# Kernel tuning notes

Measured on AMD Instinct MI355X. Metric: run time of the kernel, lower is better.

## Reference

```python
import jax, jax.numpy as jnp
from jax import lax
import numpy as np

DN = ('NCHW', 'OIHW', 'NCHW')
LEAKY_SLOPE = 0.01  # torch nn.LeakyReLU default


def conv(x, w, b=None, stride=1, pad=0):
    y = lax.conv_general_dilated(x, w, (stride, stride), [(pad, pad), (pad, pad)],
                                 dimension_numbers=DN)
    return y if b is None else y + b[None, :, None, None]


def conv_transpose2d(x, w, b):
    # torch ConvTranspose2d(k=4, s=2, p=1); w layout (Cin, Cout, 4, 4)
    wf = jnp.transpose(jnp.flip(w, (2, 3)), (1, 0, 2, 3))  # -> OIHW
    y = lax.conv_general_dilated(x, wf, (1, 1), [(2, 2), (2, 2)],
                                 lhs_dilation=(2, 2), dimension_numbers=DN)
    return y + b[None, :, None, None]


def residual_stack(x, rw3, rw1):
    # 6 ResidualLayers: x + conv1x1(relu(conv3x3(x))), both convs bias-free
    for i in range(rw3.shape[0]):
        h = jax.nn.relu(conv(x, rw3[i], pad=1))
        x = x + conv(h, rw1[i])
    return x


def vector_quantize(latents, codebook):
    # latents: [B, D, H, W] -> NHWC
    lat = jnp.transpose(latents, (0, 2, 3, 1))
    B, H, W, D = lat.shape
    flat = lat.reshape(-1, D)  # [N, D]
    # pairwise squared distances [N, K]
    dist = (jnp.sum(flat ** 2, axis=1, keepdims=True)
            + jnp.sum(codebook ** 2, axis=1)
            - 2.0 * flat @ codebook.T)
    inds = jnp.argmin(dist, axis=1)            # [N]
    q = codebook[inds].reshape(B, H, W, D)     # gather == one-hot matmul
    commitment_loss = jnp.mean((lax.stop_gradient(q) - lat) ** 2)
    embedding_loss = jnp.mean((q - lax.stop_gradient(lat)) ** 2)
    q_st = lat + lax.stop_gradient(q - lat)    # straight-through
    return jnp.transpose(q_st, (0, 3, 1, 2)), embedding_loss, commitment_loss


def setup_inputs() -> dict:
    key = jax.random.key(0)
    ks = iter(jax.random.split(key, 32))
    B, C, S = 16, 3, 128
    H0, H1 = 128, 256          # hidden_dims
    D, K = 64, 512             # embedding_dim, num_embeddings
    n_res = 6

    def w(shape, scale=0.05):
        return (jax.random.normal(next(ks), shape, dtype=jnp.float32) * scale)

    inp = {
        'x': jax.random.normal(next(ks), (B, C, S, S), dtype=jnp.float32),
        # encoder
        'ew0': w((H0, C, 4, 4)), 'eb0': jnp.zeros((H0,), jnp.float32),
        'ew1': w((H1, H0, 4, 4)), 'eb1': jnp.zeros((H1,), jnp.float32),
        'ew2': w((H1, H1, 3, 3)), 'eb2': jnp.zeros((H1,), jnp.float32),
        'erw3': w((n_res, H1, H1, 3, 3)),
        'erw1': w((n_res, H1, H1, 1, 1)),
        'ew3': w((D, H1, 1, 1)), 'eb3': jnp.zeros((D,), jnp.float32),
        # codebook, uniform(-1/K, 1/K) as in torch init
        'codebook': jax.random.uniform(next(ks), (K, D), jnp.float32, -1.0 / K, 1.0 / K),
        # decoder
        'dw0': w((H1, D, 3, 3)), 'db0': jnp.zeros((H1,), jnp.float32),
        'drw3': w((n_res, H1, H1, 3, 3)),
        'drw1': w((n_res, H1, H1, 1, 1)),
        'tw0': w((H1, H0, 4, 4)), 'tb0': jnp.zeros((H0,), jnp.float32),
        'tw1': w((H0, C, 4, 4)), 'tb1': jnp.zeros((C,), jnp.float32),
    }
    return inp


def reference(x, ew0, eb0, ew1, eb1, ew2, eb2, erw3, erw1, ew3, eb3,
              codebook, dw0, db0, drw3, drw1, tw0, tb0, tw1, tb1):
    lrelu = lambda t: jax.nn.leaky_relu(t, LEAKY_SLOPE)
    # encoder: two stride-2 downsamples, conv3x3, 6 residuals, 1x1 -> D
    h = lrelu(conv(x, ew0, eb0, stride=2, pad=1))   # [B,128,64,64]
    h = lrelu(conv(h, ew1, eb1, stride=2, pad=1))   # [B,256,32,32]
    h = lrelu(conv(h, ew2, eb2, stride=1, pad=1))
    h = residual_stack(h, erw3, erw1)
    h = lrelu(h)
    z = lrelu(conv(h, ew3, eb3))                    # [B,64,32,32]
    # vector quantization
    q, embedding_loss, commitment_loss = vector_quantize(z, codebook)
    # decoder
    d = lrelu(conv(q, dw0, db0, stride=1, pad=1))   # [B,256,32,32]
    d = residual_stack(d, drw3, drw1)
    d = lrelu(d)
    d = lrelu(conv_transpose2d(d, tw0, tb0))        # [B,128,64,64]
    recons = jnp.tanh(conv_transpose2d(d, tw1, tb1))  # [B,3,128,128]
    return recons, embedding_loss, commitment_loss
```

## Files before the change

### kernel.cpp

```cpp
#include <hip/hip_runtime.h>
#include <math.h>


typedef __attribute__((ext_vector_type(8))) short bf16x8;
typedef __attribute__((ext_vector_type(4))) float f32x4;

__device__ __forceinline__ float bf2f(short s) {
    unsigned u = ((unsigned)(unsigned short)s) << 16;
    return __builtin_bit_cast(float, u);
}
__device__ __forceinline__ unsigned short f2bfu(float f) {
    unsigned u = __builtin_bit_cast(unsigned, f);
    u = (u + 0x7fff + ((u >> 16) & 1)) >> 16;
    return (unsigned short)u;
}
__device__ __forceinline__ short f2bf(float f) { return (short)f2bfu(f); }

template<int ACT>
__device__ __forceinline__ float actf(float v) {
    if (ACT == 1) return fmaxf(v, 0.f);
    if (ACT == 2) return v > 0.f ? v : 0.01f * v;
    return v;
}

__device__ __forceinline__ void gload_lds16(const void* g, void* l) {
    __builtin_amdgcn_global_load_lds(
        (const __attribute__((address_space(1))) unsigned int*)g,
        (__attribute__((address_space(3))) unsigned int*)l, 16, 0, 0);
}

__device__ __forceinline__ int fof(int r) { return (r & 3) ^ ((r >> 2) & 3); }

#define WAITV(N) asm volatile("s_waitcnt vmcnt(" #N ")" ::: "memory")

__global__ __launch_bounds__(256) void prep_perm_k(const float* __restrict__ src,
        short* __restrict__ dst, int COUT, int CIN, int T, int total) {
    int i = blockIdx.x * 256 + threadIdx.x;
    if (i >= total) return;
    int ic = i % CIN; int r = i / CIN;
    int oc = r % COUT; r /= COUT;
    int t = r % T; int c = r / T;
    dst[i] = f2bf(src[(((size_t)c * COUT + oc) * CIN + ic) * T + t]);
}

__global__ __launch_bounds__(256) void prep_tw0_k(const float* __restrict__ src,
        short* __restrict__ dst) {
    int i = blockIdx.x * 256 + threadIdx.x;
    if (i >= 4 * 4 * 128 * 256) return;
    int ic = i & 255; int r = i >> 8;
    int oc = r & 127; r >>= 7;
    int tap = r & 3; int par = r >> 2;
    int py = par >> 1, px = par & 1, my = tap >> 1, mx = tap & 1;
    int ky = 2 * my + (py ^ 1), kx = 2 * mx + (px ^ 1);
    dst[i] = f2bf(src[(((size_t)ic * 128 + oc) * 4 + ky) * 4 + kx]);
}

template<int CIN, int NTAPS, int TAPPAT, int SM, int INW, int OUTACT,
         bool HASB, bool FUSE>
__global__ __launch_bounds__(512, 1) void rconv_k(
        const short* __restrict__ in, const short* __restrict__ Wp,
        const float* __restrict__ bias, const short* __restrict__ W1p,
        short* __restrict__ outp) {
    constexpr int CH64 = (CIN >= 128) ? CIN / 64 : 1;
    constexpr int LG2 = (CH64 == 4) ? 2 : (CH64 == 2) ? 1 : 0;
    constexpr int ST = NTAPS * CH64;
    __shared__ short sLds[FUSE ? 77824 : 61440];
    const int tid = threadIdx.x;
    const int lane = tid & 63, wv = tid >> 6;
    const int wr = wv >> 2, wc = wv & 3;
    const int pix0 = blockIdx.x * 64;
    const int l15 = lane & 15, hi = lane >> 4;
    const int sl = (hi ^ fof(l15)) * 8;

    const int arow = (tid >> 2) & 63, akk = tid >> 8, aslot = tid & 3;
    const short* Aptr;
    {
        int pixa = pix0 + arow;
        int ba = pixa >> 10, Ya = (pixa >> 5) & 31, Xa = pixa & 31;
        Aptr = in + (size_t)((ba * INW + SM * Ya + 2) * INW + (SM * Xa + 2)) * CIN
                  + akk * 32 + (aslot ^ fof(arow)) * 8;
    }
    const short* Bptr[4];
#pragma unroll
    for (int j = 0; j < 4; j++) {
        int gb = tid + 512 * j;
        int kkb = gb >> 10, oc = (gb >> 2) & 255, slb = gb & 3;
        Bptr[j] = Wp + (size_t)oc * CIN + kkb * 32 + ((slb ^ fof(oc)) * 8);
    }

    auto stage = [&](int s, int bi) {
        int t = s >> LG2;
        int c0 = (s & (CH64 - 1)) * 64;
        int rof, cof;
        if (TAPPAT == 1) { rof = t / 3 - 1; cof = t % 3 - 1; }
        else             { rof = (t >> 2) - 1; cof = (t & 3) - 1; }
        int aoff = (rof * INW + cof) * CIN + c0;
        int woff = t * (256 * CIN) + c0;
        char* L = (char*)sLds + bi * 40960;
        gload_lds16(Aptr + aoff, L + tid * 16);
#pragma unroll
        for (int j = 0; j < 4; j++)
            gload_lds16(Bptr[j] + woff, L + 8192 + (tid + 512 * j) * 16);
    };

    f32x4 acc[2][4];
#pragma unroll
    for (int mi = 0; mi < 2; mi++)
#pragma unroll
        for (int ni = 0; ni < 4; ni++) acc[mi][ni] = f32x4{0.f, 0.f, 0.f, 0.f};

    stage(0, 0);
    stage(1, 1);
    int bi = 0;
    for (int s = 0; s < ST; ++s) {
        if (s < ST - 1) { WAITV(5); } else { WAITV(0); }
        __builtin_amdgcn_s_barrier();
        int nx = bi + 2; if (nx >= 3) nx -= 3;
        if (s + 2 < ST) stage(s + 2, nx);
        const short* L = sLds + bi * 20480;
        const short* LB = L + 4096;
        bf16x8 af[2][2], bfr[4][2];
#pragma unroll
        for (int kk = 0; kk < 2; kk++) {
#pragma unroll
            for (int mi = 0; mi < 2; mi++)
                af[mi][kk] = *(const bf16x8*)(L + kk * 2048
                    + (wr * 32 + mi * 16 + l15) * 32 + sl);
#pragma unroll
            for (int ni = 0; ni < 4; ni++)
                bfr[ni][kk] = *(const bf16x8*)(LB + kk * 8192
                    + (wc * 64 + ni * 16 + l15) * 32 + sl);
        }
        __builtin_amdgcn_s_setprio(1);
#pragma unroll
        for (int kk = 0; kk < 2; kk++)
#pragma unroll
            for (int mi = 0; mi < 2; mi++)
#pragma unroll
                for (int ni = 0; ni < 4; ni++)
                    acc[mi][ni] = __builtin_amdgcn_mfma_f32_16x16x32_bf16(
                        af[mi][kk], bfr[ni][kk], acc[mi][ni], 0, 0, 0);
        __builtin_amdgcn_s_setprio(0);
        bi = (bi == 2) ? 0 : bi + 1;
    }

    if (!FUSE) {
#pragma unroll
        for (int mi = 0; mi < 2; mi++)
#pragma unroll
            for (int r = 0; r < 4; r++) {
                int lrow = wr * 32 + mi * 16 + hi * 4 + r;
                int pix = pix0 + lrow;
                int b = pix >> 10, Y = (pix >> 5) & 31, X = pix & 31;
                size_t base = (((size_t)b * 36 + Y + 2) * 36 + X + 2) * 256;
#pragma unroll
                for (int ni = 0; ni < 4; ni++) {
                    int col = wc * 64 + ni * 16 + l15;
                    float v = acc[mi][ni][r];
                    if (HASB) v += bias[col];
                    outp[base + col] = f2bf(actf<OUTACT>(v));
                }
            }
        return;
    }

    short* H = sLds + 61440;
#pragma unroll
    for (int mi = 0; mi < 2; mi++)
#pragma unroll
        for (int r = 0; r < 4; r++) {
            int lrow = wr * 32 + mi * 16 + hi * 4 + r;
            int frow = fof(lrow);
#pragma unroll
            for (int ni = 0; ni < 4; ni++) {
                int col = wc * 64 + ni * 16 + l15;
                H[((col >> 5) * 64 + lrow) * 32 + (((col >> 3) & 3) ^ frow) * 8
                  + (col & 7)] = f2bf(fmaxf(acc[mi][ni][r], 0.f));
            }
        }

    const short* W1ptr[4];
#pragma unroll
    for (int j = 0; j < 4; j++) {
        int gb = tid + 512 * j;
        int kkb = gb >> 10, oc = (gb >> 2) & 255, slb = gb & 3;
        W1ptr[j] = W1p + (size_t)oc * 256 + kkb * 32 + ((slb ^ fof(oc)) * 8);
    }
    auto stage2 = [&](int s2, int bb) {
        char* L = (char*)sLds + bb * 40960 + 8192;
#pragma unroll
        for (int j = 0; j < 4; j++)
            gload_lds16(W1ptr[j] + s2 * 64, L + (tid + 512 * j) * 16);
    };
    stage2(0, 0);
    stage2(1, 1);
    __syncthreads();

    f32x4 acc2[2][4];
#pragma unroll
    for (int mi = 0; mi < 2; mi++)
#pragma unroll
        for (int ni = 0; ni < 4; ni++) acc2[mi][ni] = f32x4{0.f, 0.f, 0.f, 0.f};

    for (int s2 = 0; s2 < 4; ++s2) {
        if (s2 < 3) { WAITV(4); } else { WAITV(0); }
        __builtin_amdgcn_s_barrier();
        if (s2 == 0) stage2(2, 2);
        if (s2 == 1) stage2(3, 0);
        const short* LB = sLds + ((s2 < 3) ? s2 : 0) * 20480 + 4096;
        bf16x8 af2[2][2], bf2r[4][2];
#pragma unroll
        for (int kk = 0; kk < 2; kk++) {
            int ck = s2 * 2 + kk;
#pragma unroll
            for (int mi = 0; mi < 2; mi++)
                af2[mi][kk] = *(const bf16x8*)(H
                    + (ck * 64 + wr * 32 + mi * 16 + l15) * 32 + sl);
#pragma unroll
            for (int ni = 0; ni < 4; ni++)
                bf2r[ni][kk] = *(const bf16x8*)(LB + kk * 8192
                    + (wc * 64 + ni * 16 + l15) * 32 + sl);
        }
        __builtin_amdgcn_s_setprio(1);
#pragma unroll
        for (int kk = 0; kk < 2; kk++)
#pragma unroll
            for (int mi = 0; mi < 2; mi++)
#pragma unroll
                for (int ni = 0; ni < 4; ni++)
                    acc2[mi][ni] = __builtin_amdgcn_mfma_f32_16x16x32_bf16(
                        af2[mi][kk], bf2r[ni][kk], acc2[mi][ni], 0, 0, 0);
        __builtin_amdgcn_s_setprio(0);
    }
#pragma unroll
    for (int mi = 0; mi < 2; mi++)
#pragma unroll
        for (int r = 0; r < 4; r++) {
            int lrow = wr * 32 + mi * 16 + hi * 4 + r;
            int pix = pix0 + lrow;
            int b = pix >> 10, Y = (pix >> 5) & 31, X = pix & 31;
            size_t base = (((size_t)b * 36 + Y + 2) * 36 + X + 2) * 256;
#pragma unroll
            for (int ni = 0; ni < 4; ni++) {
                int col = wc * 64 + ni * 16 + l15;
                float v = acc2[mi][ni][r] + bf2f(in[base + col]);
                outp[base + col] = f2bf(actf<OUTACT>(v));
            }
        }
}

template<int CIN, int COUT, int NTAPS, int TAPPAT, int SM, int INW,
         int OUTACT, bool RES, bool HASB, int OUTMODE, int BN>
__global__ __launch_bounds__(256) void gconv_k(
        const short* __restrict__ in, const short* __restrict__ Wp,
        const float* __restrict__ bias, const short* __restrict__ res,
        void* __restrict__ outp) {
    constexpr int KCH = CIN / 32;
    constexpr int LG = (KCH == 8) ? 3 : (KCH == 4) ? 2 : (KCH == 2) ? 1 : 0;
    constexpr int ST = NTAPS * KCH;
    constexpr int NF = BN / 32;
    constexpr int WN = BN / 2;
    __shared__ short sA[3 * 128 * 32];
    __shared__ short sB[3 * BN * 32];
    const int tid = threadIdx.x;
    const int lane = tid & 63, wv = tid >> 6;
    const int wr = wv >> 1, wc = wv & 1;
    const int pix0 = blockIdx.x * 128;
    const int oc0 = blockIdx.y * BN;
    int py = 0, px = 0;
    if (TAPPAT == 3) {
        int par = blockIdx.z;
        py = par >> 1; px = par & 1;
        Wp += (size_t)par * NTAPS * COUT * CIN;
    }

    const int sp = tid >> 2;
    const int fsp = fof(sp);
    const int swz = ((tid & 3) ^ fsp) * 8;
    int rbA[2];
#pragma unroll
    for (int rd = 0; rd < 2; rd++) {
        int pix = pix0 + sp + rd * 64;
        int b = pix >> 10, Y = (pix >> 5) & 31, X = pix & 31;
        rbA[rd] = ((b * INW + SM * Y + 2) * INW + (SM * X + 2)) * CIN + swz;
    }
    const int wb0 = (oc0 + sp) * CIN + swz;
    const int wb1 = (oc0 + sp + 64) * CIN + swz;

    f32x4 acc[4][NF];
#pragma unroll
    for (int i = 0; i < 4; i++)
#pragma unroll
        for (int j = 0; j < NF; j++) acc[i][j] = f32x4{0.f, 0.f, 0.f, 0.f};

    const int sslot = ((lane >> 4) ^ fof(lane & 15)) * 8;
    const int abase = (wr * 64 + (lane & 15)) * 32 + sslot;
    const int bbase = (wc * WN + (lane & 15)) * 32 + sslot;

    auto stage = [&](int s, int biq) {
        int t = s >> LG, c = s & (KCH - 1);
        int rof, cof;
        if (TAPPAT == 0) { rof = 0; cof = 0; }
        else if (TAPPAT == 1) { rof = t / 3 - 1; cof = t % 3 - 1; }
        else if (TAPPAT == 2) { rof = t / 4 - 1; cof = t % 4 - 1; }
        else { int my = t >> 1, mx = t & 1;
               rof = (py == 0) ? -my : 1 - my;
               cof = (px == 0) ? -mx : 1 - mx; }
        const int tapoff = (rof * INW + cof) * CIN + c * 32;
        char* a = (char*)sA + biq * 8192;
        char* b = (char*)sB + biq * (BN * 64);
        const short* wt = Wp + (size_t)t * COUT * CIN + c * 32;
        gload_lds16(in + rbA[0] + tapoff, a + tid * 16);
        gload_lds16(in + rbA[1] + tapoff, a + 4096 + tid * 16);
        gload_lds16(wt + wb0, b + tid * 16);
        if (BN == 128) gload_lds16(wt + wb1, b + 4096 + tid * 16);
    };

    stage(0, 0);
    stage(1, 1);
    int cur = 0;
    for (int s = 0; s < ST; ++s) {
        if (s < ST - 1) {
            if (BN == 128) { WAITV(4); } else { WAITV(3); }
        } else {
            WAITV(0);
        }
        __builtin_amdgcn_s_barrier();
        int nxt = cur + 2; if (nxt >= 3) nxt -= 3;
        if (s + 2 < ST) stage(s + 2, nxt);
        const short* a = sA + cur * 4096;
        const short* b = sB + cur * (BN * 32);
        bf16x8 af[4], bfm[NF];
#pragma unroll
        for (int mi = 0; mi < 4; mi++)
            af[mi] = *(const bf16x8*)(a + abase + mi * 512);
#pragma unroll
        for (int ni = 0; ni < NF; ni++)
            bfm[ni] = *(const bf16x8*)(b + bbase + ni * 512);
        __builtin_amdgcn_s_setprio(1);
#pragma unroll
        for (int mi = 0; mi < 4; mi++)
#pragma unroll
            for (int ni = 0; ni < NF; ni++)
                acc[mi][ni] = __builtin_amdgcn_mfma_f32_16x16x32_bf16(
                    af[mi], bfm[ni], acc[mi][ni], 0, 0, 0);
        __builtin_amdgcn_s_setprio(0);
        cur = (cur == 2) ? 0 : cur + 1;
    }
#pragma unroll
    for (int mi = 0; mi < 4; mi++) {
#pragma unroll
        for (int r = 0; r < 4; r++) {
            int pix = pix0 + wr * 64 + mi * 16 + (lane >> 4) * 4 + r;
            int b = pix >> 10, Y = (pix >> 5) & 31, X = pix & 31;
            size_t rowoff = 0;
            if (OUTMODE == 0)
                rowoff = (((size_t)b * 36 + Y + 2) * 36 + X + 2) * COUT;
            else if (OUTMODE == 2)
                rowoff = (((size_t)b * 68 + 2 * Y + py + 2) * 68 + 2 * X + px + 2) * 128;
#pragma unroll
            for (int ni = 0; ni < NF; ni++) {
                int col = oc0 + wc * WN + ni * 16 + (lane & 15);
                float v = acc[mi][ni][r];
                if (HASB) v += bias[col];
                if (OUTMODE == 1) {
                    ((float*)outp)[(size_t)pix * COUT + col] = actf<OUTACT>(v);
                } else {
                    size_t off = rowoff + col;
                    if (RES) v += bf2f(res[off]);
                    ((short*)outp)[off] = f2bf(actf<OUTACT>(v));
                }
            }
        }
    }
}

__global__ __launch_bounds__(256) void conv0_k(const float* __restrict__ x,
        const float* __restrict__ W, const float* __restrict__ bias,
        short* __restrict__ P0) {
    __shared__ float sIn[3 * 18 * 66];
    __shared__ float sW[48 * 32];
    int b = blockIdx.z, ocg = blockIdx.y, tile = blockIdx.x;
    int y0 = (tile >> 1) * 8, x0 = (tile & 1) * 32;
    int tid = threadIdx.x;
    for (int t = tid; t < 1536; t += 256) {
        int k = t >> 5, oc = t & 31;
        sW[t] = W[(size_t)(ocg * 32 + oc) * 48 + k];
    }
    for (int t = tid; t < 3 * 18 * 66; t += 256) {
        int ic = t / 1188; int rem = t - ic * 1188;
        int ry = rem / 66, rx = rem - ry * 66;
        int iy = 2 * y0 - 1 + ry, ix = 2 * x0 - 1 + rx;
        float v = 0.f;
        if ((unsigned)iy < 128u && (unsigned)ix < 128u)
            v = x[((size_t)b * 3 + ic) * 16384 + iy * 128 + ix];
        sIn[t] = v;
    }
    __syncthreads();
    int r = tid >> 5, cx = tid & 31;
    float acc[32];
#pragma unroll
    for (int o = 0; o < 32; o++) acc[o] = 0.f;
#pragma unroll
    for (int ic = 0; ic < 3; ic++) {
#pragma unroll
        for (int k = 0; k < 16; k++) {
            int ky = k >> 2, kx = k & 3;
            float xv = sIn[ic * 1188 + (2 * r + ky) * 66 + 2 * cx + kx];
            const float4* wp = (const float4*)(sW + (ic * 16 + k) * 32);
#pragma unroll
            for (int q = 0; q < 8; q++) {
                float4 w = wp[q];
                acc[4 * q + 0] += w.x * xv; acc[4 * q + 1] += w.y * xv;
                acc[4 * q + 2] += w.z * xv; acc[4 * q + 3] += w.w * xv;
            }
        }
    }
    size_t base = (((size_t)b * 68 + y0 + r + 2) * 68 + x0 + cx + 2) * 128 + ocg * 32;
#pragma unroll
    for (int q = 0; q < 16; q++) {
        float v0 = actf<2>(acc[2 * q] + bias[ocg * 32 + 2 * q]);
        float v1 = actf<2>(acc[2 * q + 1] + bias[ocg * 32 + 2 * q + 1]);
        ((int*)(P0 + base))[q] = (int)f2bfu(v0) | ((int)f2bfu(v1) << 16);
    }
}

__global__ __launch_bounds__(256) void vq_argmin_k(const float* __restrict__ zr,
        const float* __restrict__ cb, int* __restrict__ ind) {
    __shared__ short sZ[2][128 * 32];
    __shared__ short sC[2][128 * 32];
    __shared__ float sN[128];
    const int tid = threadIdx.x;
    const int lane = tid & 63, wv = tid >> 6;
    const int pos0 = blockIdx.x * 128;
#pragma unroll
    for (int it = 0; it < 4; ++it) {
        int task = tid + it * 256;
        int row = task >> 3, kq = task & 7;
        const float4* zp = (const float4*)(zr + (size_t)(pos0 + row) * 64 + kq * 8);
        float4 v0 = zp[0], v1 = zp[1];
        int slot = ((kq & 3) ^ fof(row)) * 8;
        short tmp[8] = {f2bf(v0.x), f2bf(v0.y), f2bf(v0.z), f2bf(v0.w),
                        f2bf(v1.x), f2bf(v1.y), f2bf(v1.z), f2bf(v1.w)};
        *(bf16x8*)&sZ[kq >> 2][row * 32 + slot] = *(bf16x8*)tmp;
    }
    const int sslot = ((lane >> 4) ^ fof(lane & 15)) * 8;
    const int l15 = lane & 15;
    float best[2][4]; int bidx[2][4];
#pragma unroll
    for (int mi = 0; mi < 2; mi++)
#pragma unroll
        for (int r = 0; r < 4; r++) { best[mi][r] = INFINITY; bidx[mi][r] = 0; }
    for (int ch = 0; ch < 4; ++ch) {
        __syncthreads();
#pragma unroll
        for (int it = 0; it < 4; ++it) {
            int task = tid + it * 256;
            int row = task >> 3, kq = task & 7;
            const float4* cp = (const float4*)(cb + (size_t)(ch * 128 + row) * 64 + kq * 8);
            float4 v0 = cp[0], v1 = cp[1];
            int slot = ((kq & 3) ^ fof(row)) * 8;
            short tmp[8] = {f2bf(v0.x), f2bf(v0.y), f2bf(v0.z), f2bf(v0.w),
                            f2bf(v1.x), f2bf(v1.y), f2bf(v1.z), f2bf(v1.w)};
            *(bf16x8*)&sC[kq >> 2][row * 32 + slot] = *(bf16x8*)tmp;
        }
        if (tid < 128) {
            const float4* cp = (const float4*)(cb + (size_t)(ch * 128 + tid) * 64);
            float s = 0.f;
#pragma unroll
            for (int q = 0; q < 16; q++) {
                float4 v = cp[q];
                s += v.x * v.x + v.y * v.y + v.z * v.z + v.w * v.w;
            }
            sN[tid] = s;
        }
        __syncthreads();
        f32x4 acc[2][8];
#pragma unroll
        for (int mi = 0; mi < 2; mi++)
#pragma unroll
            for (int ni = 0; ni < 8; ni++) acc[mi][ni] = f32x4{0.f, 0.f, 0.f, 0.f};
#pragma unroll
        for (int kc = 0; kc < 2; ++kc) {
            bf16x8 za[2], ca[8];
#pragma unroll
            for (int mi = 0; mi < 2; mi++)
                za[mi] = *(const bf16x8*)&sZ[kc][(wv * 32 + mi * 16 + l15) * 32 + sslot];
#pragma unroll
            for (int ni = 0; ni < 8; ni++)
                ca[ni] = *(const bf16x8*)&sC[kc][(ni * 16 + l15) * 32 + sslot];
#pragma unroll
            for (int mi = 0; mi < 2; mi++)
#pragma unroll
                for (int ni = 0; ni < 8; ni++)
                    acc[mi][ni] = __builtin_amdgcn_mfma_f32_16x16x32_bf16(
                        za[mi], ca[ni], acc[mi][ni], 0, 0, 0);
        }
#pragma unroll
        for (int mi = 0; mi < 2; mi++)
#pragma unroll
            for (int ni = 0; ni < 8; ni++) {
                float nrm = sN[ni * 16 + l15];
                int idx = ch * 128 + ni * 16 + l15;
#pragma unroll
                for (int r = 0; r < 4; r++) {
                    float sc = nrm - 2.f * acc[mi][ni][r];
                    if (sc < best[mi][r]) { best[mi][r] = sc; bidx[mi][r] = idx; }
                }
            }
    }
#pragma unroll
    for (int m = 1; m < 16; m <<= 1) {
#pragma unroll
        for (int mi = 0; mi < 2; mi++)
#pragma unroll
            for (int r = 0; r < 4; r++) {
                float os = __shfl_xor(best[mi][r], m);
                int   oi = __shfl_xor(bidx[mi][r], m);
                if (os < best[mi][r] || (os == best[mi][r] && oi < bidx[mi][r])) {
                    best[mi][r] = os; bidx[mi][r] = oi;
                }
            }
    }
    if (l15 == 0) {
        int g = lane >> 4;
#pragma unroll
        for (int mi = 0; mi < 2; mi++)
#pragma unroll
            for (int r = 0; r < 4; r++)
                ind[pos0 + wv * 32 + mi * 16 + g * 4 + r] = bidx[mi][r];
    }
}

__global__ __launch_bounds__(256) void vq_gather_k(const float* __restrict__ zr,
        const float* __restrict__ cb, const int* __restrict__ ind,
        short* __restrict__ q, float* __restrict__ part) {
    int pos = blockIdx.x * 256 + threadIdx.x;
    int b = pos >> 10, hw = pos & 1023, y = hw >> 5, xx = hw & 31;
    int idx = ind[pos];
    const float4* cp = (const float4*)(cb + (size_t)idx * 64);
    const float4* zp = (const float4*)(zr + (size_t)pos * 64);
    size_t qb = (((size_t)b * 36 + y + 2) * 36 + xx + 2) * 64;
    float sum = 0.f;
#pragma unroll
    for (int d4 = 0; d4 < 16; d4++) {
        float4 c = cp[d4], z = zp[d4];
        float dx = c.x - z.x, dy = c.y - z.y, dz = c.z - z.z, dw = c.w - z.w;
        sum += dx * dx + dy * dy + dz * dz + dw * dw;
        ((int*)(q + qb))[2 * d4] = (int)f2bfu(c.x) | ((int)f2bfu(c.y) << 16);
        ((int*)(q + qb))[2 * d4 + 1] = (int)f2bfu(c.z) | ((int)f2bfu(c.w) << 16);
    }
#pragma unroll
    for (int m = 1; m < 64; m <<= 1) sum += __shfl_xor(sum, m);
    __shared__ float sred[4];
    int lane = threadIdx.x & 63, wvv = threadIdx.x >> 6;
    if (lane == 0) sred[wvv] = sum;
    __syncthreads();
    if (threadIdx.x == 0)
        part[blockIdx.x] = sred[0] + sred[1] + sred[2] + sred[3];
}

__global__ void finalize_k(const float* __restrict__ part, float* __restrict__ out) {
    if (threadIdx.x == 0) {
        float s = 0.f;
        for (int k = 0; k < 64; k++) s += part[k];
        float m = s / 1048576.f;
        out[786432] = m;
        out[786433] = m;
    }
}

__global__ __launch_bounds__(256) void tw1_k(const short* __restrict__ in,
        const float* __restrict__ W, const float* __restrict__ bias,
        float* __restrict__ out) {
    __shared__ float sW[16 * 128 * 4];
    int b = blockIdx.y, y0 = blockIdx.x * 8;
    int tid = threadIdx.x;
    for (int t = tid; t < 2048; t += 256) {
        int k = t >> 7, ic = t & 127;
        float4 v;
        v.x = W[((size_t)ic * 3 + 0) * 16 + k];
        v.y = W[((size_t)ic * 3 + 1) * 16 + k];
        v.z = W[((size_t)ic * 3 + 2) * 16 + k];
        v.w = 0.f;
        *(float4*)&sW[t * 4] = v;
    }
    __syncthreads();
    int r = tid >> 5, g = tid & 31;
    int oy = y0 + r, py = oy & 1, Y = oy >> 1, pxp = g & 1;
    float acc[4][3];
#pragma unroll
    for (int p = 0; p < 4; p++)
#pragma unroll
        for (int o = 0; o < 3; o++) acc[p][o] = 0.f;
#pragma unroll
    for (int my = 0; my < 2; my++) {
        int iy = Y + ((py == 0) ? -my : 1 - my) + 2;
        const short* rowp = in + (((size_t)b * 68 + iy) * 68) * 128;
        int ky = 2 * my + (py ^ 1);
#pragma unroll
        for (int mx = 0; mx < 2; mx++) {
            int kx = 2 * mx + (pxp ^ 1);
            int cof = ((pxp == 0) ? -mx : 1 - mx) + 2;
            const float* wbase = &sW[((ky * 4 + kx) * 128) * 4];
            const short* pptr[4];
#pragma unroll
            for (int p = 0; p < 4; p++) {
                int X = ((g + 32 * p) >> 1) + cof;
                pptr[p] = rowp + (size_t)X * 128;
            }
            for (int icb = 0; icb < 16; icb++) {
                bf16x8 v[4];
#pragma unroll
                for (int p = 0; p < 4; p++)
                    v[p] = *(const bf16x8*)(pptr[p] + icb * 8);
#pragma unroll
                for (int j = 0; j < 8; j++) {
                    float4 w = *(const float4*)&wbase[(icb * 8 + j) * 4];
#pragma unroll
                    for (int p = 0; p < 4; p++) {
                        float xv = bf2f(v[p][j]);
                        acc[p][0] += w.x * xv;
                        acc[p][1] += w.y * xv;
                        acc[p][2] += w.z * xv;
                    }
                }
            }
        }
    }
#pragma unroll
    for (int p = 0; p < 4; p++) {
        int ox = g + 32 * p;
#pragma unroll
        for (int o = 0; o < 3; o++)
            out[(((size_t)b * 3 + o) << 14) + oy * 128 + ox] =
                tanhf(acc[p][o] + bias[o]);
    }
}

extern "C" void kernel_launch(void* const* d_in, const int* in_sizes, int n_in,
                              void* d_out, int out_size, void* d_ws, size_t ws_size,
                              hipStream_t stream) {
    const float* x    = (const float*)d_in[0];
    const float* ew0  = (const float*)d_in[1];
    const float* eb0  = (const float*)d_in[2];
    const float* ew1  = (const float*)d_in[3];
    const float* eb1  = (const float*)d_in[4];
    const float* ew2  = (const float*)d_in[5];
    const float* eb2  = (const float*)d_in[6];
    const float* erw3 = (const float*)d_in[7];
    const float* erw1 = (const float*)d_in[8];
    const float* ew3  = (const float*)d_in[9];
    const float* eb3  = (const float*)d_in[10];
    const float* cbk  = (const float*)d_in[11];
    const float* dw0  = (const float*)d_in[12];
    const float* db0  = (const float*)d_in[13];
    const float* drw3 = (const float*)d_in[14];
    const float* drw1 = (const float*)d_in[15];
    const float* tw0  = (const float*)d_in[16];
    const float* tb0  = (const float*)d_in[17];
    const float* tw1  = (const float*)d_in[18];
    const float* tb1  = (const float*)d_in[19];
    float* out = (float*)d_out;

    short* S = (short*)d_ws;
    short* P0  = S;
    short* PB  = P0 + 9469952;
    short* PC  = PB + 5308416;
    short* Pq  = PC + 5308416;
    short* Wp1 = Pq + 1327104;
    short* We2 = Wp1 + 524288;
    short* Wer3 = We2 + 589824;
    short* We11 = Wer3 + 3538944;
    short* Wz   = We11 + 393216;
    short* Wd0  = Wz + 16384;
    short* Wdr3 = Wd0 + 147456;
    short* Wdr1 = Wdr3 + 3538944;
    short* Wt0  = Wdr1 + 393216;
    float* F   = (float*)(S + 31080448);
    float* Zr  = F;
    float* PART = Zr + 1048576;
    int*   IND = (int*)(PART + 64);

    hipMemsetAsync(d_ws, 0, (size_t)21413888 * 2, stream);

    auto gp = [](int n) { return dim3((n + 255) / 256); };
    prep_perm_k<<<gp(524288), 256, 0, stream>>>(ew1, Wp1, 256, 128, 16, 524288);
    prep_perm_k<<<gp(589824), 256, 0, stream>>>(ew2, We2, 256, 256, 9, 589824);
    prep_perm_k<<<gp(3538944), 256, 0, stream>>>(erw3, Wer3, 256, 256, 9, 3538944);
    prep_perm_k<<<gp(393216), 256, 0, stream>>>(erw1, We11, 256, 256, 1, 393216);
    prep_perm_k<<<gp(16384), 256, 0, stream>>>(ew3, Wz, 64, 256, 1, 16384);
    prep_perm_k<<<gp(147456), 256, 0, stream>>>(dw0, Wd0, 256, 64, 9, 147456);
    prep_perm_k<<<gp(3538944), 256, 0, stream>>>(drw3, Wdr3, 256, 256, 9, 3538944);
    prep_perm_k<<<gp(393216), 256, 0, stream>>>(drw1, Wdr1, 256, 256, 1, 393216);
    prep_tw0_k<<<gp(524288), 256, 0, stream>>>(tw0, Wt0);

    conv0_k<<<dim3(16, 4, 16), 256, 0, stream>>>(x, ew0, eb0, P0);
    rconv_k<128, 16, 2, 2, 68, 2, true, false>
        <<<256, 512, 0, stream>>>(P0, Wp1, eb1, nullptr, PB);
    rconv_k<256, 9, 1, 1, 36, 2, true, false>
        <<<256, 512, 0, stream>>>(PB, We2, eb2, nullptr, PC);
    for (int i = 0; i < 6; i++) {
        short* inb  = (i & 1) ? PB : PC;
        short* outb = (i & 1) ? PC : PB;
        if (i < 5)
            rconv_k<256, 9, 1, 1, 36, 0, false, true>
                <<<256, 512, 0, stream>>>(inb, Wer3 + (size_t)i * 589824,
                    nullptr, We11 + (size_t)i * 65536, outb);
        else
            rconv_k<256, 9, 1, 1, 36, 2, false, true>
                <<<256, 512, 0, stream>>>(inb, Wer3 + (size_t)i * 589824,
                    nullptr, We11 + (size_t)i * 65536, outb);
    }
    gconv_k<256, 64, 1, 0, 1, 36, 2, false, true, 1, 64>
        <<<dim3(128, 1), 256, 0, stream>>>(PC, Wz, eb3, nullptr, Zr);

    vq_argmin_k<<<128, 256, 0, stream>>>(Zr, cbk, IND);
    vq_gather_k<<<64, 256, 0, stream>>>(Zr, cbk, IND, Pq, PART);

    rconv_k<64, 9, 1, 1, 36, 2, true, false>
        <<<256, 512, 0, stream>>>(Pq, Wd0, db0, nullptr, PC);
    for (int i = 0; i < 6; i++) {
        short* inb  = (i & 1) ? PB : PC;
        short* outb = (i & 1) ? PC : PB;
        if (i < 5)
            rconv_k<256, 9, 1, 1, 36, 0, false, true>
                <<<256, 512, 0, stream>>>(inb, Wdr3 + (size_t)i * 589824,
                    nullptr, Wdr1 + (size_t)i * 65536, outb);
        else
            rconv_k<256, 9, 1, 1, 36, 2, false, true>
                <<<256, 512, 0, stream>>>(inb, Wdr3 + (size_t)i * 589824,
                    nullptr, Wdr1 + (size_t)i * 65536, outb);
    }
    gconv_k<256, 128, 4, 3, 1, 36, 2, false, true, 2, 128>
        <<<dim3(128, 1, 4), 256, 0, stream>>>(PC, Wt0, tb0, nullptr, P0);
    tw1_k<<<dim3(16, 16), 256, 0, stream>>>(P0, tw1, tb1, out);

    finalize_k<<<1, 64, 0, stream>>>(PART, out);
}
```

Measured before the change: 632.1 us.

## Double rconv pixel tile to 128 rows and restructure conv0 per output row

```diff
diff --git a/kernel.cpp b/kernel.cpp
--- a/kernel.cpp
+++ b/kernel.cpp
@@ -32,6 +32,7 @@
 __device__ __forceinline__ int fof(int r) { return (r & 3) ^ ((r >> 2) & 3); }
 
 #define WAITV(N) asm volatile("s_waitcnt vmcnt(" #N ")" ::: "memory")
+#define LGKM0 asm volatile("s_waitcnt lgkmcnt(0)" ::: "memory")
 
 __global__ __launch_bounds__(256) void prep_perm_k(const float* __restrict__ src,
         short* __restrict__ dst, int COUT, int CIN, int T, int total) {
@@ -64,21 +65,21 @@
     constexpr int CH64 = (CIN >= 128) ? CIN / 64 : 1;
     constexpr int LG2 = (CH64 == 4) ? 2 : (CH64 == 2) ? 1 : 0;
     constexpr int ST = NTAPS * CH64;
-    __shared__ short sLds[FUSE ? 77824 : 61440];
+    __shared__ short sLds[73728];
     const int tid = threadIdx.x;
     const int lane = tid & 63, wv = tid >> 6;
     const int wr = wv >> 2, wc = wv & 3;
-    const int pix0 = blockIdx.x * 64;
+    const int pix0 = blockIdx.x * 128;
     const int l15 = lane & 15, hi = lane >> 4;
     const int sl = (hi ^ fof(l15)) * 8;
 
-    const int arow = (tid >> 2) & 63, akk = tid >> 8, aslot = tid & 3;
+    const int arow = tid >> 2, aslot = tid & 3;
     const short* Aptr;
     {
         int pixa = pix0 + arow;
         int ba = pixa >> 10, Ya = (pixa >> 5) & 31, Xa = pixa & 31;
         Aptr = in + (size_t)((ba * INW + SM * Ya + 2) * INW + (SM * Xa + 2)) * CIN
-                  + akk * 32 + (aslot ^ fof(arow)) * 8;
+                  + (aslot ^ fof(arow)) * 8;
     }
     const short* Bptr[4];
 #pragma unroll
@@ -95,17 +96,18 @@
         if (TAPPAT == 1) { rof = t / 3 - 1; cof = t % 3 - 1; }
         else             { rof = (t >> 2) - 1; cof = (t & 3) - 1; }
         int aoff = (rof * INW + cof) * CIN + c0;
+        char* L = (char*)sLds + bi * 49152;
+        gload_lds16(Aptr + aoff, L + tid * 16);
+        gload_lds16(Aptr + aoff + 32, L + 8192 + tid * 16);
         int woff = t * (256 * CIN) + c0;
-        char* L = (char*)sLds + bi * 40960;
-        gload_lds16(Aptr + aoff, L + tid * 16);
 #pragma unroll
         for (int j = 0; j < 4; j++)
-            gload_lds16(Bptr[j] + woff, L + 8192 + (tid + 512 * j) * 16);
+            gload_lds16(Bptr[j] + woff, L + 16384 + (tid + 512 * j) * 16);
     };
 
-    f32x4 acc[2][4];
-#pragma unroll
-    for (int mi = 0; mi < 2; mi++)
+    f32x4 acc[4][4];
+#pragma unroll
+    for (int mi = 0; mi < 4; mi++)
 #pragma unroll
         for (int ni = 0; ni < 4; ni++) acc[mi][ni] = f32x4{0.f, 0.f, 0.f, 0.f};
 
@@ -113,43 +115,41 @@
     stage(1, 1);
     int bi = 0;
     for (int s = 0; s < ST; ++s) {
-        if (s < ST - 1) { WAITV(5); } else { WAITV(0); }
+        if (s < ST - 1) { WAITV(6); } else { WAITV(0); }
         __builtin_amdgcn_s_barrier();
         int nx = bi + 2; if (nx >= 3) nx -= 3;
         if (s + 2 < ST) stage(s + 2, nx);
-        const short* L = sLds + bi * 20480;
-        const short* LB = L + 4096;
-        bf16x8 af[2][2], bfr[4][2];
+        const short* L = sLds + bi * 24576;
 #pragma unroll
         for (int kk = 0; kk < 2; kk++) {
-#pragma unroll
-            for (int mi = 0; mi < 2; mi++)
-                af[mi][kk] = *(const bf16x8*)(L + kk * 2048
-                    + (wr * 32 + mi * 16 + l15) * 32 + sl);
+            bf16x8 af[4], bfr[4];
+#pragma unroll
+            for (int mi = 0; mi < 4; mi++)
+                af[mi] = *(const bf16x8*)(L + kk * 4096
+                    + (wr * 64 + mi * 16 + l15) * 32 + sl);
 #pragma unroll
             for (int ni = 0; ni < 4; ni++)
-                bfr[ni][kk] = *(const bf16x8*)(LB + kk * 8192
+                bfr[ni] = *(const bf16x8*)(L + 8192 + kk * 8192
                     + (wc * 64 + ni * 16 + l15) * 32 + sl);
-        }
-        __builtin_amdgcn_s_setprio(1);
-#pragma unroll
-        for (int kk = 0; kk < 2; kk++)
-#pragma unroll
-            for (int mi = 0; mi < 2; mi++)
+            __builtin_amdgcn_s_setprio(1);
+#pragma unroll
+            for (int mi = 0; mi < 4; mi++)
 #pragma unroll
                 for (int ni = 0; ni < 4; ni++)
                     acc[mi][ni] = __builtin_amdgcn_mfma_f32_16x16x32_bf16(
-                        af[mi][kk], bfr[ni][kk], acc[mi][ni], 0, 0, 0);
-        __builtin_amdgcn_s_setprio(0);
+                        af[mi], bfr[ni], acc[mi][ni], 0, 0, 0);
+            __builtin_amdgcn_s_setprio(0);
+        }
+        LGKM0;
         bi = (bi == 2) ? 0 : bi + 1;
     }
 
     if (!FUSE) {
 #pragma unroll
-        for (int mi = 0; mi < 2; mi++)
+        for (int mi = 0; mi < 4; mi++)
 #pragma unroll
             for (int r = 0; r < 4; r++) {
-                int lrow = wr * 32 + mi * 16 + hi * 4 + r;
+                int lrow = wr * 64 + mi * 16 + hi * 4 + r;
                 int pix = pix0 + lrow;
                 int b = pix >> 10, Y = (pix >> 5) & 31, X = pix & 31;
                 size_t base = (((size_t)b * 36 + Y + 2) * 36 + X + 2) * 256;
@@ -164,21 +164,22 @@
         return;
     }
 
-    short* H = sLds + 61440;
-#pragma unroll
-    for (int mi = 0; mi < 2; mi++)
+    __builtin_amdgcn_s_barrier();
+    short* H = sLds;
+#pragma unroll
+    for (int mi = 0; mi < 4; mi++)
 #pragma unroll
         for (int r = 0; r < 4; r++) {
-            int lrow = wr * 32 + mi * 16 + hi * 4 + r;
+            int lrow = wr * 64 + mi * 16 + hi * 4 + r;
             int frow = fof(lrow);
 #pragma unroll
             for (int ni = 0; ni < 4; ni++) {
                 int col = wc * 64 + ni * 16 + l15;
-                H[((col >> 5) * 64 + lrow) * 32 + (((col >> 3) & 3) ^ frow) * 8
-                  + (col & 7)] = f2bf(fmaxf(acc[mi][ni][r], 0.f));
-            }
-        }
-
+                H[(((col >> 5) * 128) + lrow) * 32
+                  + ((((col >> 3) & 3) ^ frow) * 8) + (col & 7)] =
+                    f2bf(fmaxf(acc[mi][ni][r], 0.f));
+            }
+        }
     const short* W1ptr[4];
 #pragma unroll
     for (int j = 0; j < 4; j++) {
@@ -186,46 +187,46 @@
         int kkb = gb >> 10, oc = (gb >> 2) & 255, slb = gb & 3;
         W1ptr[j] = W1p + (size_t)oc * 256 + kkb * 32 + ((slb ^ fof(oc)) * 8);
     }
-    auto stage2 = [&](int s2, int bb) {
-        char* L = (char*)sLds + bb * 40960 + 8192;
+    auto stage2 = [&](int c) {
+        char* L = (char*)sLds + 65536 + (c & 1) * 32768;
 #pragma unroll
         for (int j = 0; j < 4; j++)
-            gload_lds16(W1ptr[j] + s2 * 64, L + (tid + 512 * j) * 16);
+            gload_lds16(W1ptr[j] + c * 64, L + (tid + 512 * j) * 16);
     };
-    stage2(0, 0);
-    stage2(1, 1);
-    __syncthreads();
-
-    f32x4 acc2[2][4];
-#pragma unroll
-    for (int mi = 0; mi < 2; mi++)
+    stage2(0);
+    stage2(1);
+    LGKM0;
+
+    f32x4 acc2[4][4];
+#pragma unroll
+    for (int mi = 0; mi < 4; mi++)
 #pragma unroll
         for (int ni = 0; ni < 4; ni++) acc2[mi][ni] = f32x4{0.f, 0.f, 0.f, 0.f};
 
     for (int s2 = 0; s2 < 4; ++s2) {
         if (s2 < 3) { WAITV(4); } else { WAITV(0); }
         __builtin_amdgcn_s_barrier();
-        if (s2 == 0) stage2(2, 2);
-        if (s2 == 1) stage2(3, 0);
-        const short* LB = sLds + ((s2 < 3) ? s2 : 0) * 20480 + 4096;
-        bf16x8 af2[2][2], bf2r[4][2];
+        const short* LB = sLds + 32768 + (s2 & 1) * 16384;
+        bf16x8 af2[4][2], bf2r[4][2];
 #pragma unroll
         for (int kk = 0; kk < 2; kk++) {
-            int ck = s2 * 2 + kk;
-#pragma unroll
-            for (int mi = 0; mi < 2; mi++)
+#pragma unroll
+            for (int mi = 0; mi < 4; mi++)
                 af2[mi][kk] = *(const bf16x8*)(H
-                    + (ck * 64 + wr * 32 + mi * 16 + l15) * 32 + sl);
+                    + ((s2 * 2 + kk) * 128 + wr * 64 + mi * 16 + l15) * 32 + sl);
 #pragma unroll
             for (int ni = 0; ni < 4; ni++)
                 bf2r[ni][kk] = *(const bf16x8*)(LB + kk * 8192
                     + (wc * 64 + ni * 16 + l15) * 32 + sl);
         }
+        LGKM0;
+        __builtin_amdgcn_s_barrier();
+        if (s2 < 2) stage2(s2 + 2);
         __builtin_amdgcn_s_setprio(1);
 #pragma unroll
         for (int kk = 0; kk < 2; kk++)
 #pragma unroll
-            for (int mi = 0; mi < 2; mi++)
+            for (int mi = 0; mi < 4; mi++)
 #pragma unroll
                 for (int ni = 0; ni < 4; ni++)
                     acc2[mi][ni] = __builtin_amdgcn_mfma_f32_16x16x32_bf16(
@@ -233,10 +234,10 @@
         __builtin_amdgcn_s_setprio(0);
     }
 #pragma unroll
-    for (int mi = 0; mi < 2; mi++)
+    for (int mi = 0; mi < 4; mi++)
 #pragma unroll
         for (int r = 0; r < 4; r++) {
-            int lrow = wr * 32 + mi * 16 + hi * 4 + r;
+            int lrow = wr * 64 + mi * 16 + hi * 4 + r;
             int pix = pix0 + lrow;
             int b = pix >> 10, Y = (pix >> 5) & 31, X = pix & 31;
             size_t base = (((size_t)b * 36 + Y + 2) * 36 + X + 2) * 256;
@@ -273,10 +274,8 @@
         py = par >> 1; px = par & 1;
         Wp += (size_t)par * NTAPS * COUT * CIN;
     }
-
     const int sp = tid >> 2;
-    const int fsp = fof(sp);
-    const int swz = ((tid & 3) ^ fsp) * 8;
+    const int swz = ((tid & 3) ^ fof(sp)) * 8;
     int rbA[2];
 #pragma unroll
     for (int rd = 0; rd < 2; rd++) {
@@ -345,6 +344,7 @@
                 acc[mi][ni] = __builtin_amdgcn_mfma_f32_16x16x32_bf16(
                     af[mi], bfm[ni], acc[mi][ni], 0, 0, 0);
         __builtin_amdgcn_s_setprio(0);
+        LGKM0;
         cur = (cur == 2) ? 0 : cur + 1;
     }
 #pragma unroll
@@ -378,50 +378,56 @@
 __global__ __launch_bounds__(256) void conv0_k(const float* __restrict__ x,
         const float* __restrict__ W, const float* __restrict__ bias,
         short* __restrict__ P0) {
-    __shared__ float sIn[3 * 18 * 66];
-    __shared__ float sW[48 * 32];
-    int b = blockIdx.z, ocg = blockIdx.y, tile = blockIdx.x;
-    int y0 = (tile >> 1) * 8, x0 = (tile & 1) * 32;
+    __shared__ float sIn[3 * 4 * 130];
+    __shared__ float sW[48 * 4 * 36];
+    int y = blockIdx.x, b = blockIdx.y;
     int tid = threadIdx.x;
-    for (int t = tid; t < 1536; t += 256) {
-        int k = t >> 5, oc = t & 31;
-        sW[t] = W[(size_t)(ocg * 32 + oc) * 48 + k];
-    }
-    for (int t = tid; t < 3 * 18 * 66; t += 256) {
-        int ic = t / 1188; int rem = t - ic * 1188;
-        int ry = rem / 66, rx = rem - ry * 66;
-        int iy = 2 * y0 - 1 + ry, ix = 2 * x0 - 1 + rx;
+    for (int t = tid; t < 6144; t += 256) {
+        int k = t >> 7, oc = t & 127;
+        sW[(k * 4 + (oc >> 5)) * 36 + (oc & 31)] = W[(size_t)oc * 48 + k];
+    }
+    for (int t = tid; t < 1560; t += 256) {
+        int ic = t / 520; int rem = t - ic * 520;
+        int ry = rem / 130, rx = rem - ry * 130;
+        int iy = 2 * y - 1 + ry, ix = rx - 1;
         float v = 0.f;
         if ((unsigned)iy < 128u && (unsigned)ix < 128u)
             v = x[((size_t)b * 3 + ic) * 16384 + iy * 128 + ix];
         sIn[t] = v;
     }
     __syncthreads();
-    int r = tid >> 5, cx = tid & 31;
+    int p = tid >> 2, g = tid & 3, oc0 = g * 32;
     float acc[32];
 #pragma unroll
-    for (int o = 0; o < 32; o++) acc[o] = 0.f;
-#pragma unroll
-    for (int ic = 0; ic < 3; ic++) {
-#pragma unroll
-        for (int k = 0; k < 16; k++) {
-            int ky = k >> 2, kx = k & 3;
-            float xv = sIn[ic * 1188 + (2 * r + ky) * 66 + 2 * cx + kx];
-            const float4* wp = (const float4*)(sW + (ic * 16 + k) * 32);
-#pragma unroll
-            for (int q = 0; q < 8; q++) {
-                float4 w = wp[q];
-                acc[4 * q + 0] += w.x * xv; acc[4 * q + 1] += w.y * xv;
-                acc[4 * q + 2] += w.z * xv; acc[4 * q + 3] += w.w * xv;
-            }
-        }
-    }
-    size_t base = (((size_t)b * 68 + y0 + r + 2) * 68 + x0 + cx + 2) * 128 + ocg * 32;
-#pragma unroll
-    for (int q = 0; q < 16; q++) {
-        float v0 = actf<2>(acc[2 * q] + bias[ocg * 32 + 2 * q]);
-        float v1 = actf<2>(acc[2 * q + 1] + bias[ocg * 32 + 2 * q + 1]);
-        ((int*)(P0 + base))[q] = (int)f2bfu(v0) | ((int)f2bfu(v1) << 16);
+    for (int o = 0; o < 32; o++) acc[o] = bias[oc0 + o];
+#pragma unroll
+    for (int ic = 0; ic < 3; ic++)
+#pragma unroll
+        for (int ky = 0; ky < 4; ky++) {
+            const float* ib = sIn + ic * 520 + ky * 130 + 2 * p;
+#pragma unroll
+            for (int kx = 0; kx < 4; kx++) {
+                float xv = ib[kx];
+                const float* wr_ = sW + ((ic * 16 + ky * 4 + kx) * 4 + g) * 36;
+#pragma unroll
+                for (int q = 0; q < 8; q++) {
+                    float4 w = *(const float4*)(wr_ + q * 4);
+                    acc[4 * q + 0] += w.x * xv; acc[4 * q + 1] += w.y * xv;
+                    acc[4 * q + 2] += w.z * xv; acc[4 * q + 3] += w.w * xv;
+                }
+            }
+        }
+    size_t base = (((size_t)b * 68 + y + 2) * 68 + p + 2) * 128 + oc0;
+#pragma unroll
+    for (int q4 = 0; q4 < 4; q4++) {
+        int pk[4];
+#pragma unroll
+        for (int j = 0; j < 4; j++) {
+            float v0 = actf<2>(acc[q4 * 8 + 2 * j]);
+            float v1 = actf<2>(acc[q4 * 8 + 2 * j + 1]);
+            pk[j] = (int)f2bfu(v0) | ((int)f2bfu(v1) << 16);
+        }
+        *(int4*)(P0 + base + q4 * 8) = *(int4*)pk;
     }
 }
 
@@ -695,21 +701,21 @@
     prep_perm_k<<<gp(393216), 256, 0, stream>>>(drw1, Wdr1, 256, 256, 1, 393216);
     prep_tw0_k<<<gp(524288), 256, 0, stream>>>(tw0, Wt0);
 
-    conv0_k<<<dim3(16, 4, 16), 256, 0, stream>>>(x, ew0, eb0, P0);
+    conv0_k<<<dim3(64, 16), 256, 0, stream>>>(x, ew0, eb0, P0);
     rconv_k<128, 16, 2, 2, 68, 2, true, false>
-        <<<256, 512, 0, stream>>>(P0, Wp1, eb1, nullptr, PB);
+        <<<128, 512, 0, stream>>>(P0, Wp1, eb1, nullptr, PB);
     rconv_k<256, 9, 1, 1, 36, 2, true, false>
-        <<<256, 512, 0, stream>>>(PB, We2, eb2, nullptr, PC);
+        <<<128, 512, 0, stream>>>(PB, We2, eb2, nullptr, PC);
     for (int i = 0; i < 6; i++) {
         short* inb  = (i & 1) ? PB : PC;
         short* outb = (i & 1) ? PC : PB;
         if (i < 5)
             rconv_k<256, 9, 1, 1, 36, 0, false, true>
-                <<<256, 512, 0, stream>>>(inb, Wer3 + (size_t)i * 589824,
+                <<<128, 512, 0, stream>>>(inb, Wer3 + (size_t)i * 589824,
                     nullptr, We11 + (size_t)i * 65536, outb);
         else
             rconv_k<256, 9, 1, 1, 36, 2, false, true>
-                <<<256, 512, 0, stream>>>(inb, Wer3 + (size_t)i * 589824,
+                <<<128, 512, 0, stream>>>(inb, Wer3 + (size_t)i * 589824,
                     nullptr, We11 + (size_t)i * 65536, outb);
     }
     gconv_k<256, 64, 1, 0, 1, 36, 2, false, true, 1, 64>
@@ -719,17 +725,17 @@
     vq_gather_k<<<64, 256, 0, stream>>>(Zr, cbk, IND, Pq, PART);
 
     rconv_k<64, 9, 1, 1, 36, 2, true, false>
-        <<<256, 512, 0, stream>>>(Pq, Wd0, db0, nullptr, PC);
+        <<<128, 512, 0, stream>>>(Pq, Wd0, db0, nullptr, PC);
     for (int i = 0; i < 6; i++) {
         short* inb  = (i & 1) ? PB : PC;
         short* outb = (i & 1) ? PC : PB;
         if (i < 5)
             rconv_k<256, 9, 1, 1, 36, 0, false, true>
-                <<<256, 512, 0, stream>>>(inb, Wdr3 + (size_t)i * 589824,
+                <<<128, 512, 0, stream>>>(inb, Wdr3 + (size_t)i * 589824,
                     nullptr, Wdr1 + (size_t)i * 65536, outb);
         else
             rconv_k<256, 9, 1, 1, 36, 2, false, true>
-                <<<256, 512, 0, stream>>>(inb, Wdr3 + (size_t)i * 589824,
+                <<<128, 512, 0, stream>>>(inb, Wdr3 + (size_t)i * 589824,
                     nullptr, Wdr1 + (size_t)i * 65536, outb);
     }
     gconv_k<256, 128, 4, 3, 1, 36, 2, false, true, 2, 128>
```

Result: slower. 818.4 us (+29.5%).
